# Kernel optimization log

Measured on AMD Instinct MI355X. Metric: run time of the kernel, lower is better.

## Reference

```python
import jax, jax.numpy as jnp
import numpy as np
from jax import lax

BLANK = 27
NEG = -1e30  # safe -inf substitute (avoids NaN grads through logaddexp)


def _joint_log_probs(enc, dec, We, Wd, bf, Wp, bp):
    # Concat-then-Linear == sum of per-branch matmuls: [e;d] @ Wf = e@We + d@Wd.
    f = jnp.einsum('bte,eh->bth', enc, We)          # [B,T,H]
    g = jnp.einsum('bud,dh->buh', dec, Wd)          # [B,U1,H]
    h = jnp.tanh(f[:, :, None, :] + g[:, None, :, :] + bf)  # [B,T,U1,H]
    logits = jnp.einsum('btuh,hv->btuv', h, Wp) + bp         # [B,T,U1,V]
    return jax.nn.log_softmax(logits, axis=-1)


def _rnnt_loss_one(lp, tgt, t_len, u_len):
    # lp: [T,U1,V] log-probs, tgt: [U] int labels, t_len/u_len: scalars.
    T, U1, V = lp.shape
    blank_lp = lp[:, :, BLANK]                                   # [T,U1]
    lab_lp = jnp.take_along_axis(lp[:, :U1 - 1, :],
                                 tgt[None, :, None], axis=2)[..., 0]  # [T,U]

    # alpha[0,:] : only label emissions along u at t=0.
    alpha0 = jnp.concatenate([jnp.zeros((1,), lp.dtype),
                              jnp.cumsum(lab_lp[0])])            # [U1]

    def step(prev_alpha, inp):
        b_prev, lab_t = inp                       # [U1], [U]
        from_below = prev_alpha + b_prev          # blank move from t-1
        first = from_below[0]

        def inner(carry, x):
            fb, lab = x
            new = jnp.logaddexp(fb, carry + lab)  # blank-from-below vs label-from-left
            return new, new

        _, rest = lax.scan(inner, first, (from_below[1:], lab_t))
        alpha_t = jnp.concatenate([first[None], rest])
        return alpha_t, alpha_t

    _, alphas = lax.scan(step, alpha0, (blank_lp[:-1], lab_lp[1:]))
    alpha = jnp.concatenate([alpha0[None], alphas], axis=0)      # [T,U1]

    # Terminal: emit final blank at (t_len-1, u_len).
    return -(alpha[t_len - 1, u_len] + blank_lp[t_len - 1, u_len])


def setup_inputs() -> dict:
    key = jax.random.key(0)
    ks = jax.random.split(key, 10)
    B, T, U, E, D, H, V = 8, 400, 60, 256, 256, 512, 28
    enc_state = jax.random.normal(ks[0], (B, T, E), jnp.float32)
    dec_state = jax.random.normal(ks[1], (B, U + 1, D), jnp.float32)
    targets = jax.random.randint(ks[2], (B, U), 0, BLANK, jnp.int32)
    inputs_length = jax.random.randint(ks[3], (B,), 200, T + 1, jnp.int32)
    targets_length = jax.random.randint(ks[4], (B,), 30, U + 1, jnp.int32)
    s1 = 1.0 / np.sqrt(E + D)
    s2 = 1.0 / np.sqrt(H)
    We = jax.random.normal(ks[5], (E, H), jnp.float32) * s1
    Wd = jax.random.normal(ks[6], (D, H), jnp.float32) * s1
    bf = jax.random.normal(ks[7], (H,), jnp.float32) * s1
    Wp = jax.random.normal(ks[8], (H, V), jnp.float32) * s2
    bp = jax.random.normal(ks[9], (V,), jnp.float32) * s2
    return {"enc_state": enc_state, "dec_state": dec_state,
            "We": We, "Wd": Wd, "bf": bf, "Wp": Wp, "bp": bp,
            "targets": targets, "inputs_length": inputs_length,
            "targets_length": targets_length}


def reference(enc_state, dec_state, We, Wd, bf, Wp, bp,
              targets, inputs_length, targets_length):
    lp = _joint_log_probs(enc_state, dec_state, We, Wd, bf, Wp, bp)
    loss = jax.vmap(_rnnt_loss_one)(lp, targets, inputs_length, targets_length)
    return loss  # [B], reduction='none'
```

## Files before the change

### kernel.cpp

```cpp
#include <hip/hip_runtime.h>
#include <hip/hip_bf16.h>
#include <math.h>

#define NEGF (-1e30f)
#define LOG2E 1.4426950408889634f
#define LN2F 0.6931471805599453f
#define TSCALE 2.885390081777927f

typedef __attribute__((ext_vector_type(8))) short bf16x8;
typedef __attribute__((ext_vector_type(4))) float f32x4;

#define DROWS_PAD 480
#define DPITCH 64
#define CH 48

__device__ __forceinline__ unsigned short f2bf(float x) {
    __hip_bfloat16 h = __float2bfloat16(x);
    return *reinterpret_cast<unsigned short*>(&h);
}

__device__ __forceinline__ float wave_shr1(float x) {
    int i = __builtin_bit_cast(int, x);
    int r = __builtin_amdgcn_update_dpp(0, i, 0x138, 0xf, 0xf, true);
    return __builtin_bit_cast(float, r);
}

__device__ __forceinline__ float4 rcp4_nr(float4 d) {
    float4 y;
    y.x = __builtin_bit_cast(float, 0x7EF311C3 - __builtin_bit_cast(int, d.x));
    y.y = __builtin_bit_cast(float, 0x7EF311C3 - __builtin_bit_cast(int, d.y));
    y.z = __builtin_bit_cast(float, 0x7EF311C3 - __builtin_bit_cast(int, d.z));
    y.w = __builtin_bit_cast(float, 0x7EF311C3 - __builtin_bit_cast(int, d.w));
    float4 t;
    t.x = fmaf(-d.x, y.x, 2.f); t.y = fmaf(-d.y, y.y, 2.f);
    t.z = fmaf(-d.z, y.z, 2.f); t.w = fmaf(-d.w, y.w, 2.f);
    y.x *= t.x; y.y *= t.y; y.z *= t.z; y.w *= t.w;
    return y;
}

__global__ __launch_bounds__(256) void k_pack(const float* __restrict__ We,
                                              const float* __restrict__ Wd,
                                              const float* __restrict__ Wp,
                                              const float* __restrict__ bp,
                                              unsigned short* __restrict__ WeFrag,
                                              unsigned short* __restrict__ WdFrag,
                                              unsigned short* __restrict__ BfragP,
                                              float* __restrict__ csbp) {
    int gid = blockIdx.x * 256 + threadIdx.x;
    if (gid < 32768) {
        const float* W = (gid < 16384) ? We : Wd;
        unsigned short* F = (gid < 16384) ? WeFrag : WdFrag;
        int s = gid & 16383;
        int lane = s & 63;
        int c = (s >> 6) & 7;
        int nt = s >> 9;
        int n = nt * 16 + (lane & 15);
        int kbase = c * 32 + ((lane >> 4) & 3) * 8;
        unsigned short* dst = F + (size_t)s * 8;
#pragma unroll
        for (int j = 0; j < 8; ++j) dst[j] = f2bf(W[(size_t)(kbase + j) * 512 + n]);
    } else if (gid < 34816) {
        int s = gid - 32768;
        int lane = s & 63;
        int half = (s >> 6) & 1;
        int c = s >> 7;
        int n = half * 16 + (lane & 15);
        int kbase = c * 32 + (lane >> 4) * 8;
        unsigned short* dst = BfragP + (size_t)s * 8;
#pragma unroll
        for (int j = 0; j < 8; ++j) {
            float v = (n < 28) ? (-2.f * Wp[(kbase + j) * 28 + n]) : 0.f;
            dst[j] = f2bf(v);
        }
    } else if (gid < 34848) {
        int v = gid - 34816;
        float s = 0.f;
        if (v < 28) {
            for (int k = 0; k < 512; ++k) s += Wp[k * 28 + v];
            s += bp[v];
        }
        csbp[v] = s;
    }
}

__global__ __launch_bounds__(256) void k_gemm(const float* __restrict__ enc,
                                              const float* __restrict__ dec,
                                              const float* __restrict__ bfv,
                                              const unsigned short* __restrict__ WeFrag,
                                              const unsigned short* __restrict__ WdFrag,
                                              float* __restrict__ f,
                                              float* __restrict__ g) {
    const int wid = blockIdx.x * 4 + threadIdx.y;
    const int lane = threadIdx.x;
    const int m16 = lane & 15;
    const int quad = lane >> 4;

    const float* A; const unsigned short* WF; float* Out; int M, rt, ct; bool isg;
    if (wid < 1600) { A = enc; WF = WeFrag; Out = f; M = 3200; rt = wid >> 3; ct = wid & 7; isg = false; }
    else { int w2 = wid - 1600; A = dec; WF = WdFrag; Out = g; M = 488; rt = w2 >> 3; ct = w2 & 7; isg = true; }

    const int row = rt * 16 + m16;
    const float* arow = A + (size_t)min(row, M - 1) * 256 + quad * 8;

    f32x4 acc[4];
#pragma unroll
    for (int i = 0; i < 4; ++i) acc[i] = (f32x4){0.f, 0.f, 0.f, 0.f};

#pragma unroll
    for (int c = 0; c < 8; ++c) {
        float4 a0 = *(const float4*)(arow + c * 32);
        float4 a1 = *(const float4*)(arow + c * 32 + 4);
        union { unsigned short s[8]; bf16x8 v; } Af;
        Af.s[0] = f2bf(a0.x); Af.s[1] = f2bf(a0.y);
        Af.s[2] = f2bf(a0.z); Af.s[3] = f2bf(a0.w);
        Af.s[4] = f2bf(a1.x); Af.s[5] = f2bf(a1.y);
        Af.s[6] = f2bf(a1.z); Af.s[7] = f2bf(a1.w);
#pragma unroll
        for (int i = 0; i < 4; ++i) {
            int nt = ct * 4 + i;
            bf16x8 Bv = *(const bf16x8*)(WF + (size_t)((nt * 8 + c) * 64 + lane) * 8);
            acc[i] = __builtin_amdgcn_mfma_f32_16x16x32_bf16(Af.v, Bv, acc[i], 0, 0, 0);
        }
    }

#pragma unroll
    for (int i = 0; i < 4; ++i) {
        int n = ct * 64 + i * 16 + m16;
        float bv = isg ? bfv[n] : 0.f;
#pragma unroll
        for (int r = 0; r < 4; ++r) {
            int ro = rt * 16 + quad * 4 + r;
            if (ro < M) Out[(size_t)ro * 512 + n] = (acc[i][r] + bv) * TSCALE;
        }
    }
}

__global__ __launch_bounds__(512, 4) void k_cells(const float* __restrict__ f,
                                                  const float* __restrict__ g,
                                                  const unsigned short* __restrict__ Bfrag,
                                                  const float* __restrict__ csbp,
                                                  const int* __restrict__ targets,
                                                  const int* __restrict__ ilen,
                                                  const int* __restrict__ ulenp,
                                                  float2* __restrict__ pairD) {
    const int b = blockIdx.z;
    const int tlen = ilen[b];
    const int ulen = ulenp[b];
    const int t0 = blockIdx.x * 16;
    if (t0 >= tlen) return;
    if ((int)blockIdx.y * 8 > ulen) return;
    const int wave = threadIdx.y;
    const int lane = threadIdx.x;
    const int tid = wave * 64 + lane;

    __shared__ float fs[16 * 516];

    {
        const float4* src = (const float4*)(f + (size_t)(b * 400 + t0) * 512);
#pragma unroll
        for (int i = 0; i < 4; ++i) {
            int idx = tid + i * 512;
            int row = idx >> 7;
            int c4 = idx & 127;
            float4 v = src[idx];
            *(float4*)&fs[row * 516 + c4 * 4] = v;
        }
    }
    __syncthreads();

    const int quad = lane >> 4;
    const int m16 = lane & 15;
    const int u_raw = blockIdx.y * 8 + wave;
    const int u = min(u_raw, 60);
    const float* fsrow = fs + m16 * 516 + quad * 8;
    const float* gu = g + (size_t)(b * 61 + u) * 512 + quad * 8;
    const float4 one4 = make_float4(1.f, 1.f, 1.f, 1.f);

    f32x4 acc0 = {0.f, 0.f, 0.f, 0.f};
    f32x4 acc1 = {0.f, 0.f, 0.f, 0.f};

    float4 FA[2], FB[2], GA[2], GB[2];
    bf16x8 BR0[2], BR1[2];
    FA[0] = *(const float4*)(fsrow);
    FB[0] = *(const float4*)(fsrow + 4);
    GA[0] = *(const float4*)(gu);
    GB[0] = *(const float4*)(gu + 4);
    BR0[0] = *(const bf16x8*)(Bfrag + ((size_t)(0 * 64 + lane)) * 8);
    BR1[0] = *(const bf16x8*)(Bfrag + ((size_t)(1 * 64 + lane)) * 8);

#pragma unroll
    for (int c = 0; c < 16; ++c) {
        const int cu = c & 1;
        const int nx = cu ^ 1;
        if (c < 15) {
            FA[nx] = *(const float4*)(fsrow + (c + 1) * 32);
            FB[nx] = *(const float4*)(fsrow + (c + 1) * 32 + 4);
            GA[nx] = *(const float4*)(gu + (c + 1) * 32);
            GB[nx] = *(const float4*)(gu + (c + 1) * 32 + 4);
            BR0[nx] = *(const bf16x8*)(Bfrag + ((size_t)(((c + 1) * 2 + 0) * 64 + lane)) * 8);
            BR1[nx] = *(const bf16x8*)(Bfrag + ((size_t)(((c + 1) * 2 + 1) * 64 + lane)) * 8);
        }
        float4 s0 = FA[cu] + GA[cu];
        float4 s1 = FB[cu] + GB[cu];
        float4 e0, e1;
        e0.x = __builtin_amdgcn_exp2f(s0.x); e0.y = __builtin_amdgcn_exp2f(s0.y);
        e0.z = __builtin_amdgcn_exp2f(s0.z); e0.w = __builtin_amdgcn_exp2f(s0.w);
        e1.x = __builtin_amdgcn_exp2f(s1.x); e1.y = __builtin_amdgcn_exp2f(s1.y);
        e1.z = __builtin_amdgcn_exp2f(s1.z); e1.w = __builtin_amdgcn_exp2f(s1.w);
        float4 r0 = rcp4_nr(e0 + one4);
        float4 r1 = rcp4_nr(e1 + one4);
        union { unsigned short s[8]; bf16x8 v; } A;
        A.s[0] = f2bf(r0.x); A.s[1] = f2bf(r0.y);
        A.s[2] = f2bf(r0.z); A.s[3] = f2bf(r0.w);
        A.s[4] = f2bf(r1.x); A.s[5] = f2bf(r1.y);
        A.s[6] = f2bf(r1.z); A.s[7] = f2bf(r1.w);
        acc0 = __builtin_amdgcn_mfma_f32_16x16x32_bf16(A.v, BR0[cu], acc0, 0, 0, 0);
        acc1 = __builtin_amdgcn_mfma_f32_16x16x32_bf16(A.v, BR1[cu], acc1, 0, 0, 0);
    }

    const float cs0 = csbp[m16];
    const int n1 = 16 + m16;
    const bool n1v = (n1 < 28);
    const float cs1 = csbp[n1 & 31];
    int tv = targets[b * 60 + min(u, 59)];

    float res_blank[4], res_lab[4];
#pragma unroll
    for (int r = 0; r < 4; ++r) {
        float l0 = acc0[r] + cs0;
        float l1 = n1v ? (acc1[r] + cs1) : NEGF;
        float mx = fmaxf(l0, l1);
        mx = fmaxf(mx, __shfl_xor(mx, 1, 64));
        mx = fmaxf(mx, __shfl_xor(mx, 2, 64));
        mx = fmaxf(mx, __shfl_xor(mx, 4, 64));
        mx = fmaxf(mx, __shfl_xor(mx, 8, 64));
        float s = __builtin_amdgcn_exp2f((l0 - mx) * LOG2E) +
                  __builtin_amdgcn_exp2f((l1 - mx) * LOG2E);
        s += __shfl_xor(s, 1, 64);
        s += __shfl_xor(s, 2, 64);
        s += __shfl_xor(s, 4, 64);
        s += __shfl_xor(s, 8, 64);
        float lse = mx + __logf(s);
        int base = lane & 48;
        float labsrc = (tv < 16) ? l0 : l1;
        float labv = __shfl(labsrc, base | (tv & 15), 64);
        float blankv = __shfl(l1, base | 11, 64);
        res_blank[r] = (blankv - lse) * LOG2E;
        res_lab[r] = (labv - lse) * LOG2E;
    }

    if (m16 == 0 && u_raw <= 60) {
        float2* Pd = pairD + (size_t)b * (DROWS_PAD * DPITCH);
#pragma unroll
        for (int r = 0; r < 4; ++r) {
            int t = t0 + quad * 4 + r;
            if (t < tlen) {
                int d = t + u;
                float2 pr;
                pr.x = res_blank[r];
                pr.y = (u <= 59) ? res_lab[r] : NEGF;
                Pd[d * DPITCH + u] = pr;
            }
        }
    }
}

__global__ __launch_bounds__(256) void k_alpha(const float2* __restrict__ pairD,
                                               const int* __restrict__ ilen,
                                               const int* __restrict__ ulenp,
                                               float* __restrict__ out) {
    const int b = blockIdx.x;
    const int u = threadIdx.x;
    const int w = threadIdx.y;
    const float2* Pd = pairD + (size_t)b * (DROWS_PAD * DPITCH);
    const int tl = ilen[b];
    const int ul = ulenp[b];
    const int dstar = tl - 1 + ul;
    const int NCH = (dstar + CH - 1) / CH;
    const bool uok = (u <= 60);
    const bool lok = (u >= 1 && u <= 60);

    __shared__ char lbuf[2 * CH * 512];

    {
        const int tid = w * 64 + u;
        const float4* gs = (const float4*)Pd;
        float4* ld = (float4*)lbuf;
#pragma unroll
        for (int j = 0; j < 6; ++j) ld[tid + j * 256] = gs[tid + j * 256];
    }
    __syncthreads();

    float cur = (u == 0) ? 0.f : NEGF;
    float saved = NEGF, savedBlank = NEGF;

    for (int k = 0; k < NCH; ++k) {
        if (w > 0 && (k + 1) < NCH) {
            const int pt = (w - 1) * 64 + u;
            const float4* gs = (const float4*)(Pd + (size_t)(k + 1) * CH * DPITCH);
            float4* ld = (float4*)(lbuf + ((k + 1) & 1) * (CH * 512));
#pragma unroll
            for (int j = 0; j < 8; ++j)
                ld[pt + j * 192] = gs[pt + j * 192];
        }
        if (w == 0) {
            const char* base = lbuf + (k & 1) * (CH * 512);
            const int d0 = k * CH + 1;
#pragma unroll 16
            for (int r = 0; r < CH; ++r) {
                const int d = d0 + r;
                float2 v = *(const float2*)(base + r * 512 + u * 8);
                int t = d - u;
                float bv = (t >= 1 && t <= 399 && uok) ? v.x : NEGF;
                float lvn = wave_shr1(v.y);
                float lv = (lok && t >= 0 && t <= 399) ? lvn : NEGF;
                float up = wave_shr1(cur);
                float a = cur + bv;
                float c2 = up + lv;
                float mx = fmaxf(a, c2), mn = fminf(a, c2);
                float nv = mx + __log2f(1.f + __builtin_amdgcn_exp2f(mn - mx));
                bool valid = (t >= 0 && t <= 399 && uok);
                cur = valid ? nv : cur;
                saved = (d == dstar) ? cur : saved;
                savedBlank = (d == dstar) ? v.x : savedBlank;
            }
        }
        __syncthreads();
    }
    if (w == 0 && u == ul) out[b] = -(saved + savedBlank) * LN2F;
}

extern "C" void kernel_launch(void* const* d_in, const int* in_sizes, int n_in,
                              void* d_out, int out_size, void* d_ws, size_t ws_size,
                              hipStream_t stream) {
    const float* enc = (const float*)d_in[0];
    const float* dec = (const float*)d_in[1];
    const float* We  = (const float*)d_in[2];
    const float* Wd  = (const float*)d_in[3];
    const float* bf  = (const float*)d_in[4];
    const float* Wp  = (const float*)d_in[5];
    const float* bp  = (const float*)d_in[6];
    const int* targets = (const int*)d_in[7];
    const int* ilen    = (const int*)d_in[8];
    const int* ulen    = (const int*)d_in[9];
    float* out = (float*)d_out;
    float* ws = (float*)d_ws;

    float* f     = ws;
    float* g     = ws + 1638400;
    unsigned short* BfragP = (unsigned short*)(ws + 1888256);
    unsigned short* WeFrag = (unsigned short*)(ws + 1896448);
    unsigned short* WdFrag = (unsigned short*)(ws + 1961984);
    float* csbp  = ws + 2027520;
    float2* pairD = (float2*)(ws + 2027552);

    k_pack<<<137, 256, 0, stream>>>(We, Wd, Wp, bp, WeFrag, WdFrag, BfragP, csbp);

    k_gemm<<<462, dim3(64, 4, 1), 0, stream>>>(enc, dec, bf, WeFrag, WdFrag, f, g);

    dim3 gridC(25, 8, 8);
    dim3 blockC(64, 8, 1);
    k_cells<<<gridC, blockC, 0, stream>>>(f, g, BfragP, csbp, targets, ilen, ulen, pairD);

    k_alpha<<<8, dim3(64, 4, 1), 0, stream>>>(pairD, ilen, ulen, out);
}
```

Baseline: 142.6 us.

## Step RNN-T alpha recurrence two diagonals at a time and deepen joint prefetch

```diff
diff --git a/kernel.cpp b/kernel.cpp
--- a/kernel.cpp
+++ b/kernel.cpp
@@ -181,27 +181,31 @@
 
     float4 FA[2], FB[2], GA[2], GB[2];
     bf16x8 BR0[2], BR1[2];
-    FA[0] = *(const float4*)(fsrow);
-    FB[0] = *(const float4*)(fsrow + 4);
-    GA[0] = *(const float4*)(gu);
-    GB[0] = *(const float4*)(gu + 4);
-    BR0[0] = *(const bf16x8*)(Bfrag + ((size_t)(0 * 64 + lane)) * 8);
-    BR1[0] = *(const bf16x8*)(Bfrag + ((size_t)(1 * 64 + lane)) * 8);
+#pragma unroll
+    for (int c0 = 0; c0 < 2; ++c0) {
+        FA[c0] = *(const float4*)(fsrow + c0 * 32);
+        FB[c0] = *(const float4*)(fsrow + c0 * 32 + 4);
+        GA[c0] = *(const float4*)(gu + c0 * 32);
+        GB[c0] = *(const float4*)(gu + c0 * 32 + 4);
+        BR0[c0] = *(const bf16x8*)(Bfrag + ((size_t)((c0 * 2 + 0) * 64 + lane)) * 8);
+        BR1[c0] = *(const bf16x8*)(Bfrag + ((size_t)((c0 * 2 + 1) * 64 + lane)) * 8);
+    }
 
 #pragma unroll
     for (int c = 0; c < 16; ++c) {
         const int cu = c & 1;
-        const int nx = cu ^ 1;
-        if (c < 15) {
-            FA[nx] = *(const float4*)(fsrow + (c + 1) * 32);
-            FB[nx] = *(const float4*)(fsrow + (c + 1) * 32 + 4);
-            GA[nx] = *(const float4*)(gu + (c + 1) * 32);
-            GB[nx] = *(const float4*)(gu + (c + 1) * 32 + 4);
-            BR0[nx] = *(const bf16x8*)(Bfrag + ((size_t)(((c + 1) * 2 + 0) * 64 + lane)) * 8);
-            BR1[nx] = *(const bf16x8*)(Bfrag + ((size_t)(((c + 1) * 2 + 1) * 64 + lane)) * 8);
-        }
-        float4 s0 = FA[cu] + GA[cu];
-        float4 s1 = FB[cu] + GB[cu];
+        float4 fa = FA[cu], fb = FB[cu], ga = GA[cu], gb = GB[cu];
+        bf16x8 b0 = BR0[cu], b1 = BR1[cu];
+        if (c < 14) {
+            FA[cu] = *(const float4*)(fsrow + (c + 2) * 32);
+            FB[cu] = *(const float4*)(fsrow + (c + 2) * 32 + 4);
+            GA[cu] = *(const float4*)(gu + (c + 2) * 32);
+            GB[cu] = *(const float4*)(gu + (c + 2) * 32 + 4);
+            BR0[cu] = *(const bf16x8*)(Bfrag + ((size_t)(((c + 2) * 2 + 0) * 64 + lane)) * 8);
+            BR1[cu] = *(const bf16x8*)(Bfrag + ((size_t)(((c + 2) * 2 + 1) * 64 + lane)) * 8);
+        }
+        float4 s0 = fa + ga;
+        float4 s1 = fb + gb;
         float4 e0, e1;
         e0.x = __builtin_amdgcn_exp2f(s0.x); e0.y = __builtin_amdgcn_exp2f(s0.y);
         e0.z = __builtin_amdgcn_exp2f(s0.z); e0.w = __builtin_amdgcn_exp2f(s0.w);
@@ -214,8 +218,8 @@
         A.s[2] = f2bf(r0.z); A.s[3] = f2bf(r0.w);
         A.s[4] = f2bf(r1.x); A.s[5] = f2bf(r1.y);
         A.s[6] = f2bf(r1.z); A.s[7] = f2bf(r1.w);
-        acc0 = __builtin_amdgcn_mfma_f32_16x16x32_bf16(A.v, BR0[cu], acc0, 0, 0, 0);
-        acc1 = __builtin_amdgcn_mfma_f32_16x16x32_bf16(A.v, BR1[cu], acc1, 0, 0, 0);
+        acc0 = __builtin_amdgcn_mfma_f32_16x16x32_bf16(A.v, b0, acc0, 0, 0, 0);
+        acc1 = __builtin_amdgcn_mfma_f32_16x16x32_bf16(A.v, b1, acc1, 0, 0, 0);
     }
 
     const float cs0 = csbp[m16];
@@ -292,7 +296,7 @@
     __syncthreads();
 
     float cur = (u == 0) ? 0.f : NEGF;
-    float saved = NEGF, savedBlank = NEGF;
+    float saved = NEGF;
 
     for (int k = 0; k < NCH; ++k) {
         if (w > 0 && (k + 1) < NCH) {
@@ -306,28 +310,48 @@
         if (w == 0) {
             const char* base = lbuf + (k & 1) * (CH * 512);
             const int d0 = k * CH + 1;
-#pragma unroll 16
-            for (int r = 0; r < CH; ++r) {
-                const int d = d0 + r;
-                float2 v = *(const float2*)(base + r * 512 + u * 8);
-                int t = d - u;
-                float bv = (t >= 1 && t <= 399 && uok) ? v.x : NEGF;
-                float lvn = wave_shr1(v.y);
-                float lv = (lok && t >= 0 && t <= 399) ? lvn : NEGF;
-                float up = wave_shr1(cur);
-                float a = cur + bv;
-                float c2 = up + lv;
-                float mx = fmaxf(a, c2), mn = fminf(a, c2);
-                float nv = mx + __log2f(1.f + __builtin_amdgcn_exp2f(mn - mx));
-                bool valid = (t >= 0 && t <= 399 && uok);
-                cur = valid ? nv : cur;
-                saved = (d == dstar) ? cur : saved;
-                savedBlank = (d == dstar) ? v.x : savedBlank;
+#pragma unroll 8
+            for (int rp = 0; rp < CH / 2; ++rp) {
+                const int d = d0 + 2 * rp;
+                float2 v1 = *(const float2*)(base + (2 * rp) * 512 + u * 8);
+                float2 v2 = *(const float2*)(base + (2 * rp + 1) * 512 + u * 8);
+                const int t1 = d - u;
+                const int t2 = t1 + 1;
+                float bv1 = (t1 >= 1 && t1 <= 399 && uok) ? v1.x : NEGF;
+                float lv1 = (lok && t1 >= 0 && t1 <= 399) ? wave_shr1(v1.y) : NEGF;
+                float bv2 = (t2 >= 1 && t2 <= 399 && uok) ? v2.x : NEGF;
+                float lv2 = (lok && t2 >= 0 && t2 <= 399) ? wave_shr1(v2.y) : NEGF;
+                float A = bv1 + bv2;
+                float bv1s = wave_shr1(bv1);
+                float lv1s = wave_shr1(lv1);
+                float p1 = lv1 + bv2, p2 = bv1s + lv2;
+                float pmx = fmaxf(p1, p2), pmn = fminf(p1, p2);
+                float Bc = pmx + __log2f(1.f + __builtin_amdgcn_exp2f(pmn - pmx));
+                float C = lv1s + lv2;
+                float sh1 = wave_shr1(cur);
+                float sh2 = wave_shr1(sh1);
+                float a1 = cur + A;
+                float a2 = sh1 + Bc;
+                float a3 = sh2 + C;
+                float mx = fmaxf(fmaxf(a1, a2), a3);
+                float s = __builtin_amdgcn_exp2f(a1 - mx)
+                        + __builtin_amdgcn_exp2f(a2 - mx)
+                        + __builtin_amdgcn_exp2f(a3 - mx);
+                float nv = mx + __log2f(s);
+                float xa = cur + bv1;
+                float xb = sh1 + lv1;
+                float xmx = fmaxf(xa, xb), xmn = fminf(xa, xb);
+                float x = xmx + __log2f(1.f + __builtin_amdgcn_exp2f(xmn - xmx));
+                bool valid1 = (t1 >= 0 && t1 <= 399 && uok);
+                bool valid2 = (t2 >= 0 && t2 <= 399 && uok);
+                cur = valid2 ? nv : (valid1 ? x : cur);
+                saved = (d == dstar) ? x : saved;
+                saved = (d + 1 == dstar) ? nv : saved;
             }
         }
         __syncthreads();
     }
-    if (w == 0 && u == ul) out[b] = -(saved + savedBlank) * LN2F;
+    if (w == 0 && u == ul) out[b] = -(saved + Pd[dstar * DPITCH + u].x) * LN2F;
 }
 
 extern "C" void kernel_launch(void* const* d_in, const int* in_sizes, int n_in,
```

Result: slower. 163.2 us (+14.5%).
